# Kernel tuning notes

Hardware: AMD Instinct MI355X
Metric: run time of the kernel (lower is better)

The kernel has to match this reference:

```python
import jax, jax.numpy as jnp
import numpy as np

N, WIDTH, MODES, OUT_CH, N_LAYERS = 131072, 256, 512, 256, 4


def setup_inputs() -> dict:
    key = jax.random.key(0)
    ks = jax.random.split(key, 8)
    scale = 1.0 / (WIDTH * WIDTH)  # matches torch: 1/(in_channels*out_channels)
    return {
        "V": jax.random.normal(ks[0], (N, 3), dtype=jnp.float32),
        "fc0_w": jax.random.normal(ks[1], (WIDTH, 3), dtype=jnp.float32) * 0.02,
        "fc0_b": jnp.zeros((WIDTH,), dtype=jnp.float32),
        # real/imag stacked in last dim -> complex weights (4, in, out, modes)
        "sc_w": jax.random.normal(ks[2], (N_LAYERS, WIDTH, WIDTH, MODES, 2), dtype=jnp.float32) * scale,
        "fc1_w": jax.random.normal(ks[3], (128, WIDTH), dtype=jnp.float32) * 0.02,
        "fc1_b": jnp.zeros((128,), dtype=jnp.float32),
        "fc2_w": jax.random.normal(ks[4], (OUT_CH, 128), dtype=jnp.float32) * 0.02,
        "fc2_b": jnp.zeros((OUT_CH,), dtype=jnp.float32),
    }


def _spectral_conv(x, w_ri):
    # x: (b, c, n) real; w_ri: (c, o, modes, 2) real -> complex (c, o, modes)
    b, c, n = x.shape
    modes = w_ri.shape[2]
    n_freq = n // 2 + 1
    w = jax.lax.complex(w_ri[..., 0], w_ri[..., 1])
    x_ft = jnp.fft.rfft(x, axis=-1)                         # (b, c, n_freq)
    out_modes = jnp.einsum('bcm,com->bom', x_ft[:, :, :modes], w)
    out_ft = jnp.pad(out_modes, ((0, 0), (0, 0), (0, n_freq - modes)))
    return jnp.fft.irfft(out_ft, n=n, axis=-1).astype(x.dtype)


def reference(V, fc0_w, fc0_b, sc_w, fc1_w, fc1_b, fc2_w, fc2_b):
    # lift: (N,3) -> (N,width) -> (1,width,N)
    x = V @ fc0_w.T + fc0_b
    x = x.T[None, :, :]
    for i in range(N_LAYERS):
        x = _spectral_conv(x, sc_w[i])
    feat = x.mean(axis=-1)[0]                                # (width,)
    z = jnp.tanh(feat @ fc1_w.T + fc1_b) @ fc2_w.T + fc2_b   # (out_channels,)
    return z
```

## Files before the change

kernel.cpp:

```cpp
#include <hip/hip_runtime.h>
#include <math.h>


constexpr int kN = 131072;
constexpr int kWidth = 256;
constexpr int kModes = 512;
constexpr int kLayers = 4;
constexpr size_t kLayerStride = (size_t)kWidth * kWidth * kModes * 2;
constexpr int kGatherBlocks = 256;
constexpr int kVsumBlocks = 384;


__global__ __launch_bounds__(256) void stageA(const float* __restrict__ sc_w,
                                              const float* __restrict__ V,
                                              float* __restrict__ ws) {
    int b = blockIdx.x, t = threadIdx.x;
    if (b < kGatherBlocks) {
        int rem = b * 256 + t;
        const float* src = sc_w + (size_t)rem * (size_t)(kModes * 2);
        #pragma unroll
        for (int l = 0; l < kLayers; ++l) {
            ws[(size_t)l * 65536 + rem] = src[(size_t)l * kLayerStride];
        }
    } else {
        int vb = b - kGatherBlocks;
        int q = vb * 256 + t;
        const float4 v = reinterpret_cast<const float4*>(V)[q];
        int r = q % 3;
        float acc0 = 0.f, acc1 = 0.f, acc2 = 0.f;
        float a[3] = {0.f, 0.f, 0.f};
        a[r] = v.x + v.w;
        a[(r + 1) % 3] = v.y;
        a[(r + 2) % 3] = v.z;
        acc0 = a[0]; acc1 = a[1]; acc2 = a[2];
        __shared__ float sred[3][256];
        sred[0][t] = acc0; sred[1][t] = acc1; sred[2][t] = acc2;
        __syncthreads();
        for (int off = 128; off > 0; off >>= 1) {
            if (t < off) {
                sred[0][t] += sred[0][t + off];
                sred[1][t] += sred[1][t + off];
                sred[2][t] += sred[2][t + off];
            }
            __syncthreads();
        }
        if (t == 0) {
            float* partials = ws + 262144;
            partials[vb * 3 + 0] = sred[0][0];
            partials[vb * 3 + 1] = sred[1][0];
            partials[vb * 3 + 2] = sred[2][0];
        }
    }
}

__global__ __launch_bounds__(1024) void stageB(const float* __restrict__ ws,
                                               const float* __restrict__ fc0_w,
                                               const float* __restrict__ fc0_b,
                                               const float* __restrict__ fc1_w,
                                               const float* __restrict__ fc1_b,
                                               const float* __restrict__ fc2_w,
                                               const float* __restrict__ fc2_b,
                                               float* __restrict__ out) {
    __shared__ float red[1024];
    __shared__ float xbuf[256];
    __shared__ float part[4][256];
    __shared__ float S[3];
    __shared__ float hbuf[128];
    int t = threadIdx.x;
    const float* partials = ws + 262144;

    for (int j = 0; j < 3; ++j) {
        red[t] = (t < kVsumBlocks) ? partials[t * 3 + j] : 0.f;
        __syncthreads();
        for (int off = 512; off > 0; off >>= 1) {
            if (t < off) red[t] += red[t + off];
            __syncthreads();
        }
        if (t == 0) S[j] = red[0];
        __syncthreads();
    }

    if (t < 256) {
        xbuf[t] = S[0] * fc0_w[t * 3] + S[1] * fc0_w[t * 3 + 1] +
                  S[2] * fc0_w[t * 3 + 2] + (float)kN * fc0_b[t];
    }
    __syncthreads();

    int g = t >> 8, o = t & 255;
    for (int l = 0; l < kLayers; ++l) {
        const float* W = ws + (size_t)l * 65536;
        float acc = 0.f;
        int c0 = g * 64;
        #pragma unroll 8
        for (int i = 0; i < 64; ++i) {
            int c = c0 + i;
            acc += W[c * 256 + o] * xbuf[c];
        }
        part[g][o] = acc;
        __syncthreads();
        if (t < 256) xbuf[t] = part[0][t] + part[1][t] + part[2][t] + part[3][t];
        __syncthreads();
    }

    if (t < 256) xbuf[t] *= (1.0f / (float)kN);
    __syncthreads();

    {
        int j = t & 127, s = t >> 7;
        float acc = 0.f;
        int c0 = s * 32;
        #pragma unroll 8
        for (int i = 0; i < 32; ++i) acc += xbuf[c0 + i] * fc1_w[j * 256 + c0 + i];
        red[s * 128 + j] = acc;
        __syncthreads();
        if (t < 128) {
            float a = 0.f;
            #pragma unroll
            for (int s2 = 0; s2 < 8; ++s2) a += red[s2 * 128 + t];
            hbuf[t] = tanhf(a + fc1_b[t]);
        }
        __syncthreads();
    }

    {
        int k = t & 255, s = t >> 8;
        float acc = 0.f;
        int c0 = s * 32;
        #pragma unroll 8
        for (int i = 0; i < 32; ++i) acc += hbuf[c0 + i] * fc2_w[k * 128 + c0 + i];
        red[s * 256 + k] = acc;
        __syncthreads();
        if (t < 256) out[t] = red[t] + red[256 + t] + red[512 + t] + red[768 + t] + fc2_b[t];
    }
}

extern "C" void kernel_launch(void* const* d_in, const int* in_sizes, int n_in,
                              void* d_out, int out_size, void* d_ws, size_t ws_size,
                              hipStream_t stream) {
    const float* V     = (const float*)d_in[0];
    const float* fc0_w = (const float*)d_in[1];
    const float* fc0_b = (const float*)d_in[2];
    const float* sc_w  = (const float*)d_in[3];
    const float* fc1_w = (const float*)d_in[4];
    const float* fc1_b = (const float*)d_in[5];
    const float* fc2_w = (const float*)d_in[6];
    const float* fc2_b = (const float*)d_in[7];
    float* out = (float*)d_out;
    float* ws = (float*)d_ws;

    stageA<<<kGatherBlocks + kVsumBlocks, 256, 0, stream>>>(sc_w, V, ws);
    stageB<<<1, 1024, 0, stream>>>(ws, fc0_w, fc0_b, fc1_w, fc1_b, fc2_w, fc2_b, out);
}
```

Before: 36.77 us.

## Split single-block matvec chain into per-layer multi-block kernels with transposed weights

Replaces the single 1024-thread block that ran all four DC-mode matvecs and the head with separate launches: a V-sum kernel, a gather kernel that stores the weights transposed and also computes the lift, four 256-block matvec kernels and a small head kernel. The aim is to spread the serial matvec work across many CUs and make the weight reads coalesced. In exchange it goes from two launches to seven, adding launch and inter-kernel gaps on a very short workload.

```diff
diff --git a/kernel.cpp b/kernel.cpp
--- a/kernel.cpp
+++ b/kernel.cpp
@@ -3,135 +3,121 @@
 
 
 constexpr int kN = 131072;
-constexpr int kWidth = 256;
-constexpr int kModes = 512;
-constexpr int kLayers = 4;
-constexpr size_t kLayerStride = (size_t)kWidth * kWidth * kModes * 2;
+constexpr int kVsumBlocks = 384;
 constexpr int kGatherBlocks = 256;
-constexpr int kVsumBlocks = 384;
+constexpr size_t kLayerStrideF = (size_t)256 * 256 * 512 * 2;
 
+constexpr size_t WS_WT   = 0;
+constexpr size_t WS_PART = 262144;
+constexpr size_t WS_X    = 263296;
 
-__global__ __launch_bounds__(256) void stageA(const float* __restrict__ sc_w,
-                                              const float* __restrict__ V,
-                                              float* __restrict__ ws) {
+__global__ __launch_bounds__(256) void vsum(const float* __restrict__ V,
+                                            float* __restrict__ ws) {
+    int t = threadIdx.x, vb = blockIdx.x;
+    int q = vb * 256 + t;
+    const float4 v = reinterpret_cast<const float4*>(V)[q];
+    int r = q % 3;
+    float a[3] = {0.f, 0.f, 0.f};
+    a[r] = v.x + v.w;
+    a[(r + 1) % 3] = v.y;
+    a[(r + 2) % 3] = v.z;
+    __shared__ float sred[3][256];
+    sred[0][t] = a[0]; sred[1][t] = a[1]; sred[2][t] = a[2];
+    __syncthreads();
+    for (int off = 128; off > 0; off >>= 1) {
+        if (t < off) {
+            sred[0][t] += sred[0][t + off];
+            sred[1][t] += sred[1][t + off];
+            sred[2][t] += sred[2][t + off];
+        }
+        __syncthreads();
+    }
+    if (t == 0) {
+        float* partials = ws + WS_PART;
+        partials[vb * 3 + 0] = sred[0][0];
+        partials[vb * 3 + 1] = sred[1][0];
+        partials[vb * 3 + 2] = sred[2][0];
+    }
+}
+
+__global__ __launch_bounds__(256) void gather_lift(const float* __restrict__ sc_w,
+                                                   const float* __restrict__ fc0_w,
+                                                   const float* __restrict__ fc0_b,
+                                                   float* __restrict__ ws) {
     int b = blockIdx.x, t = threadIdx.x;
     if (b < kGatherBlocks) {
         int rem = b * 256 + t;
-        const float* src = sc_w + (size_t)rem * (size_t)(kModes * 2);
-        #pragma unroll
-        for (int l = 0; l < kLayers; ++l) {
-            ws[(size_t)l * 65536 + rem] = src[(size_t)l * kLayerStride];
-        }
+        int c = rem >> 8, o = rem & 255;
+        const float* src = sc_w + (size_t)rem * 1024;
+        float w0 = src[0];
+        float w1 = src[kLayerStrideF];
+        float w2 = src[2 * kLayerStrideF];
+        float w3 = src[3 * kLayerStrideF];
+        size_t dst = (size_t)o * 256 + c;
+        ws[dst]          = w0;
+        ws[65536 + dst]  = w1;
+        ws[131072 + dst] = w2;
+        ws[196608 + dst] = w3;
     } else {
-        int vb = b - kGatherBlocks;
-        int q = vb * 256 + t;
-        const float4 v = reinterpret_cast<const float4*>(V)[q];
-        int r = q % 3;
-        float acc0 = 0.f, acc1 = 0.f, acc2 = 0.f;
-        float a[3] = {0.f, 0.f, 0.f};
-        a[r] = v.x + v.w;
-        a[(r + 1) % 3] = v.y;
-        a[(r + 2) % 3] = v.z;
-        acc0 = a[0]; acc1 = a[1]; acc2 = a[2];
-        __shared__ float sred[3][256];
-        sred[0][t] = acc0; sred[1][t] = acc1; sred[2][t] = acc2;
-        __syncthreads();
-        for (int off = 128; off > 0; off >>= 1) {
-            if (t < off) {
-                sred[0][t] += sred[0][t + off];
-                sred[1][t] += sred[1][t + off];
-                sred[2][t] += sred[2][t + off];
+        __shared__ float red[256];
+        __shared__ float S[3];
+        const float* part = ws + WS_PART;
+        for (int j = 0; j < 3; ++j) {
+            float a = part[t * 3 + j] + ((t < kVsumBlocks - 256) ? part[(t + 256) * 3 + j] : 0.f);
+            red[t] = a;
+            __syncthreads();
+            for (int off = 128; off > 0; off >>= 1) {
+                if (t < off) red[t] += red[t + off];
+                __syncthreads();
             }
+            if (t == 0) S[j] = red[0];
             __syncthreads();
         }
-        if (t == 0) {
-            float* partials = ws + 262144;
-            partials[vb * 3 + 0] = sred[0][0];
-            partials[vb * 3 + 1] = sred[1][0];
-            partials[vb * 3 + 2] = sred[2][0];
-        }
+        ws[WS_X + t] = S[0] * fc0_w[t * 3] + S[1] * fc0_w[t * 3 + 1] +
+                       S[2] * fc0_w[t * 3 + 2] + (float)kN * fc0_b[t];
     }
 }
 
-__global__ __launch_bounds__(1024) void stageB(const float* __restrict__ ws,
-                                               const float* __restrict__ fc0_w,
-                                               const float* __restrict__ fc0_b,
-                                               const float* __restrict__ fc1_w,
-                                               const float* __restrict__ fc1_b,
-                                               const float* __restrict__ fc2_w,
-                                               const float* __restrict__ fc2_b,
-                                               float* __restrict__ out) {
-    __shared__ float red[1024];
-    __shared__ float xbuf[256];
-    __shared__ float part[4][256];
-    __shared__ float S[3];
-    __shared__ float hbuf[128];
-    int t = threadIdx.x;
-    const float* partials = ws + 262144;
-
-    for (int j = 0; j < 3; ++j) {
-        red[t] = (t < kVsumBlocks) ? partials[t * 3 + j] : 0.f;
-        __syncthreads();
-        for (int off = 512; off > 0; off >>= 1) {
-            if (t < off) red[t] += red[t + off];
-            __syncthreads();
-        }
-        if (t == 0) S[j] = red[0];
+__global__ __launch_bounds__(256) void matvec_dc(const float* __restrict__ Wt,
+                                                 const float* __restrict__ Xin,
+                                                 float* __restrict__ Xout) {
+    int o = blockIdx.x, t = threadIdx.x;
+    __shared__ float red[256];
+    red[t] = Wt[o * 256 + t] * Xin[t];
+    __syncthreads();
+    for (int off = 128; off > 0; off >>= 1) {
+        if (t < off) red[t] += red[t + off];
         __syncthreads();
     }
+    if (t == 0) Xout[o] = red[0];
+}
 
-    if (t < 256) {
-        xbuf[t] = S[0] * fc0_w[t * 3] + S[1] * fc0_w[t * 3 + 1] +
-                  S[2] * fc0_w[t * 3 + 2] + (float)kN * fc0_b[t];
-    }
+__global__ __launch_bounds__(256) void head(const float* __restrict__ X4,
+                                            const float* __restrict__ fc1_w,
+                                            const float* __restrict__ fc1_b,
+                                            const float* __restrict__ fc2_w,
+                                            const float* __restrict__ fc2_b,
+                                            float* __restrict__ out) {
+    __shared__ float feat[256];
+    __shared__ float hred[256];
+    __shared__ float h[128];
+    int t = threadIdx.x;
+    feat[t] = X4[t] * (1.0f / (float)kN);
     __syncthreads();
-
-    int g = t >> 8, o = t & 255;
-    for (int l = 0; l < kLayers; ++l) {
-        const float* W = ws + (size_t)l * 65536;
-        float acc = 0.f;
-        int c0 = g * 64;
-        #pragma unroll 8
-        for (int i = 0; i < 64; ++i) {
-            int c = c0 + i;
-            acc += W[c * 256 + o] * xbuf[c];
-        }
-        part[g][o] = acc;
-        __syncthreads();
-        if (t < 256) xbuf[t] = part[0][t] + part[1][t] + part[2][t] + part[3][t];
-        __syncthreads();
-    }
-
-    if (t < 256) xbuf[t] *= (1.0f / (float)kN);
-    __syncthreads();
-
     {
         int j = t & 127, s = t >> 7;
         float acc = 0.f;
-        int c0 = s * 32;
         #pragma unroll 8
-        for (int i = 0; i < 32; ++i) acc += xbuf[c0 + i] * fc1_w[j * 256 + c0 + i];
-        red[s * 128 + j] = acc;
+        for (int i = 0; i < 128; ++i) acc += feat[s * 128 + i] * fc1_w[j * 256 + s * 128 + i];
+        hred[s * 128 + j] = acc;
         __syncthreads();
-        if (t < 128) {
-            float a = 0.f;
-            #pragma unroll
-            for (int s2 = 0; s2 < 8; ++s2) a += red[s2 * 128 + t];
-            hbuf[t] = tanhf(a + fc1_b[t]);
-        }
+        if (t < 128) h[t] = tanhf(hred[t] + hred[128 + t] + fc1_b[t]);
         __syncthreads();
     }
-
-    {
-        int k = t & 255, s = t >> 8;
-        float acc = 0.f;
-        int c0 = s * 32;
-        #pragma unroll 8
-        for (int i = 0; i < 32; ++i) acc += hbuf[c0 + i] * fc2_w[k * 128 + c0 + i];
-        red[s * 256 + k] = acc;
-        __syncthreads();
-        if (t < 256) out[t] = red[t] + red[256 + t] + red[512 + t] + red[768 + t] + fc2_b[t];
-    }
+    float acc = fc2_b[t];
+    #pragma unroll 8
+    for (int i = 0; i < 128; ++i) acc += h[i] * fc2_w[t * 128 + i];
+    out[t] = acc;
 }
 
 extern "C" void kernel_launch(void* const* d_in, const int* in_sizes, int n_in,
@@ -148,6 +134,12 @@
     float* out = (float*)d_out;
     float* ws = (float*)d_ws;
 
-    stageA<<<kGatherBlocks + kVsumBlocks, 256, 0, stream>>>(sc_w, V, ws);
-    stageB<<<1, 1024, 0, stream>>>(ws, fc0_w, fc0_b, fc1_w, fc1_b, fc2_w, fc2_b, out);
+    vsum<<<kVsumBlocks, 256, 0, stream>>>(V, ws);
+    gather_lift<<<kGatherBlocks + 1, 256, 0, stream>>>(sc_w, fc0_w, fc0_b, ws);
+
+    float* X = ws + WS_X;
+    for (int l = 0; l < 4; ++l) {
+        matvec_dc<<<256, 256, 0, stream>>>(ws + (size_t)l * 65536, X + l * 256, X + (l + 1) * 256);
+    }
+    head<<<1, 256, 0, stream>>>(X + 4 * 256, fc1_w, fc1_b, fc2_w, fc2_b, out);
 }
```

Result: slower. 37.65 us (+2.4%).
